# Kernel tuning notes

Hardware: AMD Instinct MI355X
Metric: run time of the kernel (lower is better)

Reference implementation:

```python
import jax, jax.numpy as jnp
import numpy as np


def setup_inputs() -> dict:
    key = jax.random.key(0)
    k1, k2 = jax.random.split(key)
    B, V, D = 2048, 2000, 64
    # multi-hot weights in [0,1); zeros denote absent categories
    inputs = jax.random.uniform(k1, (B, V), dtype=jnp.float32)
    # embedding table, uniform(-1, 1) as in Ludwig's default initializer
    embeddings = jax.random.uniform(k2, (V, D), dtype=jnp.float32, minval=-1.0, maxval=1.0)
    return {"inputs": inputs, "embeddings": embeddings}


def reference(inputs, embeddings):
    # inputs: (B, V) float weights; embeddings: (V, D)
    V = embeddings.shape[0]
    # signed_input = sign(abs(inputs)) -> 1 where nonzero, else 0
    # multiple_hot_indexes = signed_input * arange(V)  (zeros map to row 0)
    idx = jnp.where(inputs != 0, jnp.arange(V, dtype=jnp.int32)[None, :], 0)  # (B, V)
    gathered = embeddings[idx]  # (B, V, D) — dense lookup, as in the original
    # weighted multiply + sum-reduce over the vocab axis
    out = jnp.einsum("bv,bvd->bd", inputs, gathered)  # (B, D)
    return out
```

## Files before the change

### kernel.cpp

```cpp
#include <hip/hip_runtime.h>


#define Bn 2048
#define Vn 2000
#define Dn 64
#define RW 8
#define WAVES 4
#define ROWS (RW * WAVES)
#define NCHUNK 8
#define KC (Vn / NCHUNK)
#define LDK 252

__global__ __launch_bounds__(256, 2)
void embw(const float* __restrict__ in, const float* __restrict__ emb,
          float* __restrict__ out) {
    __shared__ float lds[ROWS][LDK];
    const int lane = threadIdx.x & 63;
    const int wid  = threadIdx.x >> 6;
    const int bg   = blockIdx.x / NCHUNK;
    const int ch   = blockIdx.x - bg * NCHUNK;
    const int row0 = bg * ROWS + wid * RW;
    const int k0   = ch * KC;

    const float* gsrc = in + (size_t)row0 * Vn + k0;
#pragma unroll
    for (int r = 0; r < RW; ++r) {
        const float* src = gsrc + (size_t)r * Vn;
        float* dst = lds[wid * RW + r];
        for (int k = lane; k < KC; k += 64)
            dst[k] = src[k];
    }
    __syncthreads();

    const float* ep = emb + (size_t)k0 * Dn + lane;
    float acc[RW] = {0.f, 0.f, 0.f, 0.f, 0.f, 0.f, 0.f, 0.f};

#pragma unroll 1
    for (int k = 0; k < 248; k += 8) {
        float e[8];
#pragma unroll
        for (int u = 0; u < 8; ++u)
            e[u] = ep[(k + u) * Dn];
        float4 a[RW], b[RW];
#pragma unroll
        for (int r = 0; r < RW; ++r) {
            a[r] = *(const float4*)&lds[wid * RW + r][k];
            b[r] = *(const float4*)&lds[wid * RW + r][k + 4];
        }
#pragma unroll
        for (int r = 0; r < RW; ++r) {
            acc[r] = fmaf(a[r].x, e[0], acc[r]);
            acc[r] = fmaf(a[r].y, e[1], acc[r]);
            acc[r] = fmaf(a[r].z, e[2], acc[r]);
            acc[r] = fmaf(a[r].w, e[3], acc[r]);
            acc[r] = fmaf(b[r].x, e[4], acc[r]);
            acc[r] = fmaf(b[r].y, e[5], acc[r]);
            acc[r] = fmaf(b[r].z, e[6], acc[r]);
            acc[r] = fmaf(b[r].w, e[7], acc[r]);
        }
    }
#pragma unroll
    for (int k = 248; k < KC; ++k) {
        float e = ep[k * Dn];
#pragma unroll
        for (int r = 0; r < RW; ++r)
            acc[r] = fmaf(lds[wid * RW + r][k], e, acc[r]);
    }

#pragma unroll
    for (int r = 0; r < RW; ++r)
        atomicAdd(&out[(size_t)(row0 + r) * Dn + lane], acc[r]);
}

extern "C" void kernel_launch(void* const* d_in, const int* in_sizes, int n_in,
                              void* d_out, int out_size, void* d_ws, size_t ws_size,
                              hipStream_t stream) {
    const float* in  = (const float*)d_in[0];
    const float* emb = (const float*)d_in[1];
    float* out = (float*)d_out;

    hipMemsetAsync(out, 0, (size_t)out_size * sizeof(float), stream);

    const int grid = (Bn / ROWS) * NCHUNK;
    embw<<<grid, 256, 0, stream>>>(in, emb, out);
}
```

Measured before the change: 86.06 us.

## Split vocab into 16 chunks with per-chunk partials and separate reduce kernel

Each wave now handles 16 rows instead of 8 and the vocab is split into 16 chunks of 125. Each block writes its partial sums to workspace instead of issuing atomics, and a second kernel sums the 16 partials into the output, which replaces the memset and the atomics. Embedding loads are prefetched one step ahead in registers. The cost is an extra kernel launch, about 8 MB of partial-sum writes and reads, and higher register pressure from 16 accumulators.

Result: faster. 83.93 us (-2.5%).

```diff
diff --git a/kernel.cpp b/kernel.cpp
--- a/kernel.cpp
+++ b/kernel.cpp
@@ -4,72 +4,105 @@
 #define Bn 2048
 #define Vn 2000
 #define Dn 64
-#define RW 8
+#define RW 16
 #define WAVES 4
 #define ROWS (RW * WAVES)
-#define NCHUNK 8
-#define KC (Vn / NCHUNK)
-#define LDK 252
+#define KCH 16
+#define KC 125
+#define LDK 128
 
 __global__ __launch_bounds__(256, 2)
-void embw(const float* __restrict__ in, const float* __restrict__ emb,
-          float* __restrict__ out) {
+void embw_part(const float* __restrict__ in, const float* __restrict__ emb,
+               float* __restrict__ part) {
     __shared__ float lds[ROWS][LDK];
     const int lane = threadIdx.x & 63;
     const int wid  = threadIdx.x >> 6;
-    const int bg   = blockIdx.x / NCHUNK;
-    const int ch   = blockIdx.x - bg * NCHUNK;
-    const int row0 = bg * ROWS + wid * RW;
+    const int bg   = blockIdx.x / KCH;
+    const int ch   = blockIdx.x - bg * KCH;
+    const int wrow = wid * RW;
+    const int row0 = bg * ROWS + wrow;
     const int k0   = ch * KC;
 
-    const float* gsrc = in + (size_t)row0 * Vn + k0;
+    {
+        const float* src = in + (size_t)row0 * Vn + k0;
 #pragma unroll
-    for (int r = 0; r < RW; ++r) {
-        const float* src = gsrc + (size_t)r * Vn;
-        float* dst = lds[wid * RW + r];
-        for (int k = lane; k < KC; k += 64)
-            dst[k] = src[k];
+        for (int r = 0; r < RW; ++r) {
+            const float* s = src + (size_t)r * Vn;
+            lds[wrow + r][lane] = s[lane];
+            if (lane < KC - 64)
+                lds[wrow + r][lane + 64] = s[lane + 64];
+        }
     }
     __syncthreads();
 
     const float* ep = emb + (size_t)k0 * Dn + lane;
-    float acc[RW] = {0.f, 0.f, 0.f, 0.f, 0.f, 0.f, 0.f, 0.f};
+    float acc[RW];
+#pragma unroll
+    for (int r = 0; r < RW; ++r) acc[r] = 0.f;
+
+    float e[8];
+#pragma unroll
+    for (int u = 0; u < 8; ++u) e[u] = ep[u * Dn];
 
 #pragma unroll 1
-    for (int k = 0; k < 248; k += 8) {
-        float e[8];
+    for (int k = 0; k < 112; k += 8) {
+        float en[8];
 #pragma unroll
-        for (int u = 0; u < 8; ++u)
-            e[u] = ep[(k + u) * Dn];
-        float4 a[RW], b[RW];
+        for (int u = 0; u < 8; ++u) en[u] = ep[(k + 8 + u) * Dn];
 #pragma unroll
         for (int r = 0; r < RW; ++r) {
-            a[r] = *(const float4*)&lds[wid * RW + r][k];
-            b[r] = *(const float4*)&lds[wid * RW + r][k + 4];
+            float4 a = *(const float4*)&lds[wrow + r][k];
+            float4 b = *(const float4*)&lds[wrow + r][k + 4];
+            acc[r] = fmaf(a.x, e[0], acc[r]);
+            acc[r] = fmaf(a.y, e[1], acc[r]);
+            acc[r] = fmaf(a.z, e[2], acc[r]);
+            acc[r] = fmaf(a.w, e[3], acc[r]);
+            acc[r] = fmaf(b.x, e[4], acc[r]);
+            acc[r] = fmaf(b.y, e[5], acc[r]);
+            acc[r] = fmaf(b.z, e[6], acc[r]);
+            acc[r] = fmaf(b.w, e[7], acc[r]);
         }
 #pragma unroll
-        for (int r = 0; r < RW; ++r) {
-            acc[r] = fmaf(a[r].x, e[0], acc[r]);
-            acc[r] = fmaf(a[r].y, e[1], acc[r]);
-            acc[r] = fmaf(a[r].z, e[2], acc[r]);
-            acc[r] = fmaf(a[r].w, e[3], acc[r]);
-            acc[r] = fmaf(b[r].x, e[4], acc[r]);
-            acc[r] = fmaf(b[r].y, e[5], acc[r]);
-            acc[r] = fmaf(b[r].z, e[6], acc[r]);
-            acc[r] = fmaf(b[r].w, e[7], acc[r]);
-        }
+        for (int u = 0; u < 8; ++u) e[u] = en[u];
     }
 #pragma unroll
-    for (int k = 248; k < KC; ++k) {
-        float e = ep[k * Dn];
+    for (int r = 0; r < RW; ++r) {
+        float4 a = *(const float4*)&lds[wrow + r][112];
+        float4 b = *(const float4*)&lds[wrow + r][116];
+        acc[r] = fmaf(a.x, e[0], acc[r]);
+        acc[r] = fmaf(a.y, e[1], acc[r]);
+        acc[r] = fmaf(a.z, e[2], acc[r]);
+        acc[r] = fmaf(a.w, e[3], acc[r]);
+        acc[r] = fmaf(b.x, e[4], acc[r]);
+        acc[r] = fmaf(b.y, e[5], acc[r]);
+        acc[r] = fmaf(b.z, e[6], acc[r]);
+        acc[r] = fmaf(b.w, e[7], acc[r]);
+    }
+#pragma unroll
+    for (int k = 120; k < KC; ++k) {
+        float ee = ep[k * Dn];
 #pragma unroll
         for (int r = 0; r < RW; ++r)
-            acc[r] = fmaf(lds[wid * RW + r][k], e, acc[r]);
+            acc[r] = fmaf(lds[wrow + r][k], ee, acc[r]);
     }
 
+    float* pp = part + ((size_t)ch * Bn + row0) * Dn + lane;
 #pragma unroll
     for (int r = 0; r < RW; ++r)
-        atomicAdd(&out[(size_t)(row0 + r) * Dn + lane], acc[r]);
+        pp[(size_t)r * Dn] = acc[r];
+}
+
+__global__ __launch_bounds__(256, 2)
+void embw_reduce(const float* __restrict__ part, float* __restrict__ out) {
+    const int i = blockIdx.x * 256 + threadIdx.x;
+    const float4* p = (const float4*)part;
+    float4 s = p[i];
+#pragma unroll
+    for (int c = 1; c < KCH; ++c) {
+        float4 t = p[(size_t)c * (Bn * Dn / 4) + i];
+        s.x += t.x; s.y += t.y; s.z += t.z; s.w += t.w;
+    }
+    ((float4*)out)[i] = s;
 }
 
 extern "C" void kernel_launch(void* const* d_in, const int* in_sizes, int n_in,
@@ -77,10 +110,12 @@
                               hipStream_t stream) {
     const float* in  = (const float*)d_in[0];
     const float* emb = (const float*)d_in[1];
-    float* out = (float*)d_out;
+    float* out  = (float*)d_out;
+    float* part = (float*)d_ws;
 
-    hipMemsetAsync(out, 0, (size_t)out_size * sizeof(float), stream);
+    const int grid1 = (Bn / ROWS) * KCH;
+    embw_part<<<grid1, 256, 0, stream>>>(in, emb, part);
 
-    const int grid = (Bn / ROWS) * NCHUNK;
-    embw<<<grid, 256, 0, stream>>>(in, emb, out);
+    const int grid2 = (Bn * Dn / 4) / 256;
+    embw_reduce<<<grid2, 256, 0, stream>>>(part, out);
 }
```
